# Kernel optimization log

Hardware: AMD Instinct MI355X
Metric: run time of the kernel (lower is better)

## Reference

```python
import math
import jax, jax.numpy as jnp
import numpy as np

K = 8
D = 8
LAMBDA_PRIOR = 0.01
TRI = D * (D + 1) // 2  # 36
PHI_DIM = K + K * D + K * TRI  # 360
_ROWS, _COLS = np.tril_indices(D)


def _unpack_phi(phi):
    # phi: [M, PHI_DIM] -> pi_tilde [M,K], mu [M,K,D], L_vecs [M,K,TRI]
    M = phi.shape[0]
    pi_tilde = phi[:, :K]
    mu = phi[:, K:K + K * D].reshape(M, K, D)
    L_vecs = phi[:, K + K * D:].reshape(M, K, TRI)
    return pi_tilde, mu, L_vecs


def _L_vec_to_matrix(L_vecs):
    # L_vecs: [M,K,TRI] -> lower-triangular L [M,K,D,D]
    M, Kc, _ = L_vecs.shape
    L = jnp.zeros((M, Kc, D, D), dtype=L_vecs.dtype)
    return L.at[:, :, _ROWS, _COLS].set(L_vecs)


def _gmm_log_likelihood(phi, X):
    # phi: [M, PHI_DIM], X: [N, D] -> log_lik [M]
    pi_tilde, mu, L_vecs = _unpack_phi(phi)
    log_pi = jax.nn.log_softmax(pi_tilde, axis=-1)          # [M,K]
    L = _L_vec_to_matrix(L_vecs)                             # [M,K,D,D]
    diff = X[None, None, :, :] - mu[:, :, None, :]           # [M,K,N,D]
    diff_T = jnp.swapaxes(diff, -1, -2)                      # [M,K,D,N]
    # solve L alpha = diff_T for each (m,k); batched triangular solve
    alpha = jax.scipy.linalg.solve_triangular(L, diff_T, lower=True)  # [M,K,D,N]
    maha = jnp.sum(alpha * alpha, axis=-2)                   # [M,K,N]
    log_diag = jnp.log(jnp.clip(jnp.abs(jnp.diagonal(L, axis1=-2, axis2=-1)), 1e-8))
    log_det = 2.0 * jnp.sum(log_diag, axis=-1)               # [M,K]
    log_norm_const = -0.5 * (D * math.log(2 * math.pi) + log_det[:, :, None])
    log_gauss = log_norm_const - 0.5 * maha                  # [M,K,N]
    log_mix = jax.scipy.special.logsumexp(log_pi[:, :, None] + log_gauss, axis=1)  # [M,N]
    return jnp.sum(log_mix, axis=-1)                         # [M]


def setup_inputs() -> dict:
    key = jax.random.key(0)
    k1, k2 = jax.random.split(key)
    M, N = 32, 32768
    phi = jax.random.normal(k1, (M, PHI_DIM), dtype=jnp.float32)
    X = jax.random.normal(k2, (N, D), dtype=jnp.float32)
    return {"phi": phi, "X": X}


def reference(phi, X):
    # U(phi; X) = -log p(X|phi) + lambda_prior * ||phi||^2 / 2  -> [M]
    log_lik = _gmm_log_likelihood(phi, X)
    prior = 0.5 * jnp.sum(phi * phi, axis=-1)
    return -log_lik + LAMBDA_PRIOR * prior
```

## Files before the change

kernel.cpp:

```cpp
#include <hip/hip_runtime.h>
#include <math.h>

#define KK 8
#define DD 8
#define TRI 36
#define PHI_DIM 360
#define MM 32
#define NN 32768
#define GX 32
#define TPB 256
#define PP 4

#define LOG2E 1.4426950408889634f
#define LN2   0.6931471805599453f
#define SSCALE 0.8493218002880191f
#define INV_SSCALE 1.177410022515475f

__launch_bounds__(TPB)
__global__ void gmm_kernel(const float* __restrict__ phi, const float* __restrict__ X,
                           float* __restrict__ out) {
    __shared__ float s_par[KK][48];
    __shared__ float s_red[TPB / 64];

    const int m = blockIdx.y;
    const float* __restrict__ ph = phi + m * PHI_DIM;
    const int tid = threadIdx.x;

    if (tid < KK) {
        const int k = tid;
        #pragma unroll
        for (int i = 0; i < DD; i++) s_par[k][i] = ph[KK + k * DD + i];

        float Lrow[TRI];
        #pragma unroll
        for (int t = 0; t < TRI; t++) Lrow[t] = ph[KK + KK * DD + k * TRI + t];

        float logdet = 0.f;
        #pragma unroll
        for (int i = 0; i < DD; i++) {
            const int di = i * (i + 1) / 2 + i;
            logdet += 2.f * __logf(fmaxf(fabsf(Lrow[di]), 1e-8f));
        }
        #pragma unroll
        for (int i = 0; i < DD; i++) {
            const int di = i * (i + 1) / 2 + i;
            #pragma unroll
            for (int j = 0; j < i; j++) {
                const int t = i * (i + 1) / 2 + j;
                s_par[k][8 + t] = Lrow[t] * INV_SSCALE;
            }
            s_par[k][8 + di] = SSCALE / Lrow[di];
        }
        float mx = ph[0];
        #pragma unroll
        for (int i = 1; i < KK; i++) mx = fmaxf(mx, ph[i]);
        float se = 0.f;
        #pragma unroll
        for (int i = 0; i < KK; i++) se += __expf(ph[i] - mx);
        const float lse = mx + __logf(se);
        const float c_ln = (ph[k] - lse) - 0.5f * (8.f * 1.8378770664093453f + logdet);
        s_par[k][44] = c_ln * LOG2E;
    }

    float pr = 0.f;
    if (blockIdx.x == 0) {
        for (int j = tid; j < PHI_DIM; j += TPB) {
            float v = ph[j];
            pr = fmaf(v, v, pr);
        }
    }
    __syncthreads();

    const int n0 = blockIdx.x * (NN / GX) + tid;
    float x[PP][DD];
    #pragma unroll
    for (int p = 0; p < PP; p++) {
        const float4* xp = (const float4*)(X + (size_t)(n0 + p * TPB) * DD);
        float4 u0 = xp[0], u1 = xp[1];
        x[p][0] = u0.x; x[p][1] = u0.y; x[p][2] = u0.z; x[p][3] = u0.w;
        x[p][4] = u1.x; x[p][5] = u1.y; x[p][6] = u1.z; x[p][7] = u1.w;
    }

    float v[PP][KK];
    #pragma unroll
    for (int k = 0; k < KK; k++) {
        float cf[45];
        #pragma unroll
        for (int t = 0; t < 45; t++) cf[t] = s_par[k][t];

        #pragma unroll
        for (int p = 0; p < PP; p++) {
            float a[DD];
            float vv = cf[44];
            #pragma unroll
            for (int i = 0; i < DD; i++) {
                float t = x[p][i] - cf[i];
                #pragma unroll
                for (int j = 0; j < i; j++)
                    t = fmaf(-cf[8 + i * (i + 1) / 2 + j], a[j], t);
                a[i] = t * cf[8 + i * (i + 1) / 2 + i];
                vv = fmaf(-a[i], a[i], vv);
            }
            v[p][k] = vv;
        }
    }

    float acc2 = 0.f;
    #pragma unroll
    for (int p = 0; p < PP; p++) {
        float mx = v[p][0];
        #pragma unroll
        for (int i = 1; i < KK; i++) mx = fmaxf(mx, v[p][i]);
        float s = 0.f;
        #pragma unroll
        for (int i = 0; i < KK; i++) s += __builtin_exp2f(v[p][i] - mx);
        acc2 += mx + __builtin_log2f(s);
    }

    float contrib = fmaf(-LN2, acc2, 0.005f * pr);

    #pragma unroll
    for (int off = 32; off; off >>= 1) contrib += __shfl_down(contrib, off, 64);
    if ((tid & 63) == 0) s_red[tid >> 6] = contrib;
    __syncthreads();
    if (tid == 0) {
        float t = s_red[0] + s_red[1] + s_red[2] + s_red[3];
        atomicAdd(&out[m], t);
    }
}

extern "C" void kernel_launch(void* const* d_in, const int* in_sizes, int n_in,
                              void* d_out, int out_size, void* d_ws, size_t ws_size,
                              hipStream_t stream) {
    const float* phi = (const float*)d_in[0];
    const float* X   = (const float*)d_in[1];
    float* out = (float*)d_out;

    dim3 grid(GX, MM);
    gmm_kernel<<<grid, TPB, 0, stream>>>(phi, X, out);
}
```

Measured before the change: 70.86 us.

## Pack point pairs into float2 vectors for packed FMA and double per-thread work

Each thread now processes 8 points as 4 float2 pairs, so the triangular solve and Mahalanobis accumulation can use packed FP32 FMA instructions (v_pk_fma_f32) that do two lanes per instruction. The grid x dimension is halved so each block covers twice as many points, which also spreads the per-block parameter setup and shared-memory coefficient loads over more work. The costs are higher register pressure (16 x values plus 64 accumulators per thread), half as many blocks (512), which lowers occupancy and latency hiding, and packed FMA only paying off if the compiler emits it without extra moves for the broadcast scalars.

Result: no change. 69.93 us (-1.3%).

```diff
diff --git a/kernel.cpp b/kernel.cpp
--- a/kernel.cpp
+++ b/kernel.cpp
@@ -7,14 +7,19 @@
 #define PHI_DIM 360
 #define MM 32
 #define NN 32768
-#define GX 32
+#define GX 16
 #define TPB 256
-#define PP 4
+#define PP 8
+#define NPAIR 4
 
 #define LOG2E 1.4426950408889634f
 #define LN2   0.6931471805599453f
 #define SSCALE 0.8493218002880191f
 #define INV_SSCALE 1.177410022515475f
+
+typedef float v2f __attribute__((ext_vector_type(2)));
+
+__device__ __forceinline__ v2f splat(float s) { v2f r; r.x = s; r.y = s; return r; }
 
 __launch_bounds__(TPB)
 __global__ void gmm_kernel(const float* __restrict__ phi, const float* __restrict__ X,
@@ -72,49 +77,62 @@
     __syncthreads();
 
     const int n0 = blockIdx.x * (NN / GX) + tid;
-    float x[PP][DD];
+    v2f x[NPAIR][DD];
     #pragma unroll
-    for (int p = 0; p < PP; p++) {
-        const float4* xp = (const float4*)(X + (size_t)(n0 + p * TPB) * DD);
-        float4 u0 = xp[0], u1 = xp[1];
-        x[p][0] = u0.x; x[p][1] = u0.y; x[p][2] = u0.z; x[p][3] = u0.w;
-        x[p][4] = u1.x; x[p][5] = u1.y; x[p][6] = u1.z; x[p][7] = u1.w;
+    for (int q = 0; q < NPAIR; q++) {
+        const float4* xa = (const float4*)(X + (size_t)(n0 + (2 * q) * TPB) * DD);
+        const float4* xb = (const float4*)(X + (size_t)(n0 + (2 * q + 1) * TPB) * DD);
+        float4 a0 = xa[0], a1 = xa[1], b0 = xb[0], b1 = xb[1];
+        x[q][0].x = a0.x; x[q][0].y = b0.x;
+        x[q][1].x = a0.y; x[q][1].y = b0.y;
+        x[q][2].x = a0.z; x[q][2].y = b0.z;
+        x[q][3].x = a0.w; x[q][3].y = b0.w;
+        x[q][4].x = a1.x; x[q][4].y = b1.x;
+        x[q][5].x = a1.y; x[q][5].y = b1.y;
+        x[q][6].x = a1.z; x[q][6].y = b1.z;
+        x[q][7].x = a1.w; x[q][7].y = b1.w;
     }
 
-    float v[PP][KK];
+    v2f vk[NPAIR][KK];
     #pragma unroll
     for (int k = 0; k < KK; k++) {
         float cf[45];
         #pragma unroll
         for (int t = 0; t < 45; t++) cf[t] = s_par[k][t];
 
+        const v2f c2 = splat(cf[44]);
         #pragma unroll
-        for (int p = 0; p < PP; p++) {
-            float a[DD];
-            float vv = cf[44];
+        for (int q = 0; q < NPAIR; q++) {
+            v2f a[DD];
+            v2f vv = c2;
             #pragma unroll
             for (int i = 0; i < DD; i++) {
-                float t = x[p][i] - cf[i];
+                v2f t = x[q][i] - splat(cf[i]);
                 #pragma unroll
                 for (int j = 0; j < i; j++)
-                    t = fmaf(-cf[8 + i * (i + 1) / 2 + j], a[j], t);
-                a[i] = t * cf[8 + i * (i + 1) / 2 + i];
-                vv = fmaf(-a[i], a[i], vv);
+                    t = __builtin_elementwise_fma(splat(cf[8 + i * (i + 1) / 2 + j]), -a[j], t);
+                a[i] = t * splat(cf[8 + i * (i + 1) / 2 + i]);
+                vv = __builtin_elementwise_fma(-a[i], a[i], vv);
             }
-            v[p][k] = vv;
+            vk[q][k] = vv;
         }
     }
 
     float acc2 = 0.f;
     #pragma unroll
-    for (int p = 0; p < PP; p++) {
-        float mx = v[p][0];
+    for (int q = 0; q < NPAIR; q++) {
+        v2f mx = vk[q][0];
         #pragma unroll
-        for (int i = 1; i < KK; i++) mx = fmaxf(mx, v[p][i]);
-        float s = 0.f;
+        for (int i = 1; i < KK; i++) mx = __builtin_elementwise_max(mx, vk[q][i]);
+        v2f s = splat(0.f);
         #pragma unroll
-        for (int i = 0; i < KK; i++) s += __builtin_exp2f(v[p][i] - mx);
-        acc2 += mx + __builtin_log2f(s);
+        for (int i = 0; i < KK; i++) {
+            v2f d = vk[q][i] - mx;
+            s.x += __builtin_exp2f(d.x);
+            s.y += __builtin_exp2f(d.y);
+        }
+        acc2 += mx.x + __builtin_log2f(s.x);
+        acc2 += mx.y + __builtin_log2f(s.y);
     }
 
     float contrib = fmaf(-LN2, acc2, 0.005f * pr);
```
